# Kernel tuning notes

Measured on AMD Instinct MI355X. Metric: run time of the kernel, lower is better.

Reference implementation:

```python
import jax, jax.numpy as jnp
import numpy as np

EPS = 1e-5
NEG_SLOPE = 0.2
B, C, P, K, E, H = 16, 16, 2048, 16, 64, 2


def cross_set_gather(f, idx):
    # f: (B, C, P), idx: (B, P, K) -> (B, C, P, K)
    return jax.vmap(lambda fb, ib: fb[:, ib])(f, idx)


def bn(x, g, b, m, v, axes):
    # x normalized along channel dim; g,b,m,v shaped to broadcast via `axes` reshape
    return (x - m.reshape(axes)) * (g.reshape(axes) / jnp.sqrt(v.reshape(axes) + EPS)) + b.reshape(axes)


def setup_inputs() -> dict:
    key = jax.random.key(0)
    ks = jax.random.split(key, 16)
    features = jax.random.normal(ks[0], (B, C, P), dtype=jnp.float32)
    neighbor_indices = jax.random.randint(ks[1], (B, P, K), 0, P)
    mask = jax.random.randint(ks[2], (B, 1, P), 0, 2).astype(bool)
    s = 0.1
    return {
        "features": features,
        "neighbor_indices": neighbor_indices,
        "mask": mask,
        "node_w": jax.random.normal(ks[3], (H, E, C)) * s,
        "node_g": jnp.ones((H, E)),
        "node_b": jnp.zeros((H, E)),
        "node_m": jax.random.normal(ks[4], (H, E)) * s,
        "node_v": jax.random.uniform(ks[5], (H, E)) + 0.5,
        "edge_w": jax.random.normal(ks[6], (H, E, C)) * s,
        "edge_bias": jax.random.normal(ks[7], (H, E)) * s,
        "edge_g": jnp.ones((H, E)),
        "edge_b2": jnp.zeros((H, E)),
        "edge_m": jax.random.normal(ks[8], (H, E)) * s,
        "edge_v": jax.random.uniform(ks[9], (H, E)) + 0.5,
        "self_w": jax.random.normal(ks[10], (H, E)) * s,
        "self_b": jax.random.normal(ks[11], (H,)) * s,
        "nb_w": jax.random.normal(ks[12], (H, E)) * s,
        "nb_b": jax.random.normal(ks[13], (H,)) * s,
    }


def _forward(features, neighbor_indices, mask, node_w, node_g, node_b, node_m, node_v,
             edge_w, edge_bias, edge_g, edge_b2, edge_m, edge_v, self_w, self_b, nb_w, nb_b):
    mask_f = mask.astype(features.dtype)  # (B,1,P)
    # node encoding (Conv1d k=1 + BN): (B,H,E,P)
    nodes = jnp.einsum('hec,bcp->bhep', node_w, features)
    nodes = bn(nodes, node_g, node_b, node_m, node_v, (1, H, E, 1))
    # edge features: neighbor - center, (B,C,P,K)
    nbr = cross_set_gather(features, neighbor_indices)
    edge_feat = nbr - features[:, :, :, None]
    # edge encoding (Conv2d k=1 + BN): (B,H,E,P,K)
    enc = jnp.einsum('hec,bcpk->bhepk', edge_w, edge_feat) + edge_bias[None, :, :, None, None]
    enc = bn(enc, edge_g, edge_b2, edge_m, edge_v, (1, H, E, 1, 1))
    # attention scores
    self_score = jnp.einsum('he,bhep->bhp', self_w, nodes) + self_b[None, :, None]  # (B,H,P)
    nb_score = jnp.einsum('he,bhepk->bhpk', nb_w, enc) + nb_b[None, :, None, None]  # (B,H,P,K)
    logits = self_score[..., None] + nb_score
    logits = jnp.where(logits >= 0, logits, NEG_SLOPE * logits)  # leaky_relu(0.2)
    # neighbor validity mask: (B,P,K)
    valid = cross_set_gather(mask_f, neighbor_indices)[:, 0]
    vb = valid[:, None, :, :]  # (B,1,P,K)
    logits = jnp.where(vb == 0, -jnp.inf, logits)
    coef = jnp.nan_to_num(jax.nn.softmax(logits, axis=-1), nan=0.0, posinf=0.0, neginf=0.0)  # (B,H,P,K)
    # weighted aggregation + relu: (B,H,E,P)
    att = jax.nn.relu(jnp.einsum('bhpk,bhepk->bhep', coef, enc))
    # graph features: masked max over K
    enc_masked = jnp.where(vb[:, :, None, :, :] == 0, -jnp.inf, enc)
    graph = jnp.max(enc_masked, axis=-1)  # (B,H,E,P)
    graph = jnp.where(jnp.isinf(graph), 0.0, graph)
    # multi-head combine: element-wise max over heads, then mask
    att_out = jnp.max(att, axis=1) * mask_f  # (B,E,P)
    graph_out = jnp.max(graph, axis=1) * mask_f  # (B,E,P)
    return att_out, graph_out


def reference(features, neighbor_indices, mask, node_w, node_g, node_b, node_m, node_v,
              edge_w, edge_bias, edge_g, edge_b2, edge_m, edge_v, self_w, self_b, nb_w, nb_b):
    return _forward(features, neighbor_indices, mask, node_w, node_g, node_b, node_m, node_v,
                    edge_w, edge_bias, edge_g, edge_b2, edge_m, edge_v, self_w, self_b, nb_w, nb_b)
```

## Files before the change

kernel.cpp:

```cpp
#include <hip/hip_runtime.h>
#include <hip/hip_bf16.h>
#include <hip/hip_fp16.h>
#include <math.h>

#define NB 16
#define NC 16
#define NP 2048
#define NK 16
#define NE 64
#define NH 2
#define EPSV 1e-5f
#define NSLOPE 0.2f
#define QINV -1e30f
#define QTHR -1e29f

#define WS_SECB  12288
#define WS_CNB2  13312
#define WS_PQ    16384
#define WS_PS    278528
#define WS_EPB   2162688

__device__ __forceinline__ float ldf(const void* p, int i, int isb) {
  return isb ? __bfloat162float(((const __hip_bfloat16*)p)[i]) : ((const float*)p)[i];
}
__device__ __forceinline__ unsigned f2bf(float f) {
  unsigned u = __float_as_uint(f);
  return (u + 0x7FFFu + ((u >> 16) & 1u)) >> 16;
}
__device__ __forceinline__ float bflo(unsigned v) { return __uint_as_float(v << 16); }
__device__ __forceinline__ float bfhi(unsigned v) { return __uint_as_float(v & 0xFFFF0000u); }

__global__ void __launch_bounds__(256) k_proj(
    const void* feat, const void* mask,
    const void* edge_w, const void* node_w,
    const void* edge_g, const void* edge_v, const void* edge_bias,
    const void* edge_m, const void* edge_b2,
    const void* node_g, const void* node_v, const void* node_b, const void* node_m,
    const void* self_w, const void* self_b, const void* nb_w, const void* nb_b,
    char* ws)
{
  __shared__ int sh_isb, sh_mbyte;
  __shared__ float ewl[128*17];
  __shared__ float nwl[128*17];
  __shared__ float fl[NC][64];
  __shared__ float w2[128], wn[128], ctr[128];
  __shared__ float s_wq[32], s_wsc[32], s_cself[2];
  __shared__ unsigned char mtile[64];

  const int tid = threadIdx.x;
  const int w = tid >> 6, lane = tid & 63;

  if (w == 0) {
    const unsigned short* u = (const unsigned short*)feat;
    int cnt = 0;
#pragma unroll
    for (int i = 0; i < 8; i++) {
      int ex = (u[lane*8 + i] >> 7) & 0xFF;
      cnt += (ex >= 100 && ex <= 135) ? 1 : 0;
    }
#pragma unroll
    for (int o = 32; o >= 1; o >>= 1) cnt += __shfl_xor(cnt, o);
    if (lane == 0) sh_isb = (cnt >= 460) ? 1 : 0;
  }
  if (w == 1) {
    const unsigned char* mb = (const unsigned char*)mask;
    int c = 0;
#pragma unroll
    for (int i = 0; i < 16; i++) {
      int ix = lane*16 + i;
      c += ((ix & 3) && mb[ix]) ? 1 : 0;
    }
#pragma unroll
    for (int o = 32; o >= 1; o >>= 1) c += __shfl_xor(c, o);
    if (lane == 0) sh_mbyte = (c > 0) ? 1 : 0;
  }
  __syncthreads();
  const int isb = sh_isb, mbyte = sh_mbyte;

  const int bid = blockIdx.x;
  const int b  = (bid & 7)*2 + ((bid >> 3) & 1);
  const int pt = bid >> 4;
  const int p0 = pt * 64;

  for (int i = tid; i < 128*16; i += 256) {
    const int he = i >> 4, c = i & 15;
    ewl[he*17 + c] = ldf(edge_w, i, isb);
    nwl[he*17 + c] = ldf(node_w, i, isb);
  }
  for (int i = tid; i < NC*64; i += 256) {
    int c = i >> 6, p = i & 63;
    fl[c][p] = ldf(feat, (b*NC + c)*NP + p0 + p, isb);
  }
  if (tid < 64) {
    bool mv;
    if (mbyte) mv = ((const unsigned char*)mask)[b*NP + p0 + tid] != 0;
    else       mv = ((const int*)mask)[b*NP + p0 + tid] != 0;
    mtile[tid] = mv ? 1 : 0;
  }
  if (tid >= 64 && tid < 192) {
    const int he = tid - 64, h = he >> 6;
    float se = ldf(edge_g, he, isb) * rsqrtf(ldf(edge_v, he, isb) + EPSV);
    float cb = se * (ldf(edge_bias, he, isb) - ldf(edge_m, he, isb)) + ldf(edge_b2, he, isb);
    float ns = ldf(node_g, he, isb) * rsqrtf(ldf(node_v, he, isb) + EPSV);
    w2[he]  = ldf(nb_w, he, isb) * se;
    wn[he]  = ldf(self_w, he, isb) * ns;
    ctr[he] = ldf(self_w, he, isb) * (ldf(node_b, he, isb) - ldf(node_m, he, isb) * ns);
    if (bid == 0) {
      ((float2*)(ws + WS_SECB))[he] = make_float2(se, cb);
      float t = ldf(nb_w, he, isb) * cb;
#pragma unroll
      for (int o = 32; o >= 1; o >>= 1) t += __shfl_xor(t, o);
      if ((he & 63) == 0)
        ((float*)(ws + WS_CNB2))[h] = t + ldf(nb_b, h, isb);
    }
  }
  if (bid == 0 && tid == 0) {
    ((int*)ws)[0] = isb;
    ((int*)ws)[1] = mbyte;
  }
  __syncthreads();

  if (tid < 128) {
    const int h = tid >> 6, c = (tid >> 2) & 15, eq = tid & 3;
    float sq = 0.f, sn = 0.f;
#pragma unroll
    for (int i = 0; i < 16; i++) {
      const int e = eq*16 + i;
      sq += w2[h*NE+e] * ewl[(h*NE+e)*17 + c];
      sn += wn[h*NE+e] * nwl[(h*NE+e)*17 + c];
    }
    sq += __shfl_xor(sq, 1); sq += __shfl_xor(sq, 2);
    sn += __shfl_xor(sn, 1); sn += __shfl_xor(sn, 2);
    if (eq == 0) { s_wq[h*16 + c] = sq; s_wsc[h*16 + c] = sn; }
  }
  if (tid >= 128 && tid < 136) {
    const int h = (tid - 128) >> 2, eq = tid & 3;
    float cs = 0.f;
#pragma unroll
    for (int i = 0; i < 16; i++) cs += ctr[h*NE + eq*16 + i];
    cs += __shfl_xor(cs, 1); cs += __shfl_xor(cs, 2);
    if (eq == 0) s_cself[h] = cs + ldf(self_b, h, isb);
  }
  __syncthreads();

  const int e = tid & 63;
  const int pp = tid >> 6;
  float wv0[NC], wv1[NC];
#pragma unroll
  for (int c = 0; c < NC; c++) {
    wv0[c] = ewl[e*17 + c];
    wv1[c] = ewl[(NE + e)*17 + c];
  }
  unsigned* epb = (unsigned*)(ws + WS_EPB);
  const long base = (long)(b*NP + p0) * 64;
  for (int pass = 0; pass < 16; pass++) {
    const int p = pass*4 + pp;
    if (!mtile[p]) continue;
    float a0 = 0.f, a1 = 0.f;
#pragma unroll
    for (int c = 0; c < NC; c++) {
      const float f = fl[c][p];
      a0 = fmaf(wv0[c], f, a0);
      a1 = fmaf(wv1[c], f, a1);
    }
    epb[base + (long)p*64 + e] = f2bf(a0) | (f2bf(a1) << 16);
  }

  if (tid < 64) {
    float q0=0.f, q1=0.f, s0=0.f, s1=0.f;
#pragma unroll
    for (int c = 0; c < NC; c++) {
      const float f = fl[c][tid];
      q0 = fmaf(s_wq[c],     f, q0);
      q1 = fmaf(s_wq[16+c],  f, q1);
      s0 = fmaf(s_wsc[c],    f, s0);
      s1 = fmaf(s_wsc[16+c], f, s1);
    }
    const int p = p0 + tid;
    const bool mv = mtile[tid] != 0;
    ((float2*)(ws + WS_PQ))[b*NP + p] = make_float2(mv ? q0 : QINV, mv ? q1 : QINV);
    ((float2*)(ws + WS_PS))[b*NP + p] = make_float2(s0 + s_cself[0], s1 + s_cself[1]);
  }
}

__global__ void __launch_bounds__(256) k_main(const int* nidx, char* ws, void* out)
{
  __shared__ float sh_se[128], sh_cbe[128], sh_cnb[2];
  __shared__ uint2 ent[32][17];
  __shared__ unsigned char cntcm[32];
  __shared__ float att_t[NE][33];
  __shared__ float gr_t[NE][33];

  const int tid  = threadIdx.x;
  const int w    = tid >> 6;
  const int lane = tid & 63;

  const int isb = ((const int*)ws)[0];
  if (tid < 128) {
    const float2 sc = ((const float2*)(ws + WS_SECB))[tid];
    sh_se[tid]  = sc.x;
    sh_cbe[tid] = sc.y;
  }
  if (tid < 2) sh_cnb[tid] = ((const float*)(ws + WS_CNB2))[tid];
  __syncthreads();

  const float2* Pq = (const float2*)(ws + WS_PQ);
  const float2* Ps = (const float2*)(ws + WS_PS);
  const int bid = blockIdx.x;
  const int b  = (bid & 7)*2 + ((bid >> 3) & 1);
  const int pt = bid >> 4;
  const int p0 = pt * 32;
  const float cnb0 = sh_cnb[0], cnb1 = sh_cnb[1];

  {
    const int pl = w*8 + (lane >> 3);
    const int p  = p0 + pl;
    const int kk = (lane & 7) * 2;
    const float2 Pcq = Pq[b*NP + p];
    const float2 Pcs = Ps[b*NP + p];
    const bool cm = (Pcq.x > QTHR);
    const int2 iv = *(const int2*)(nidx + ((long)b*NP + p)*NK + kk);
    const float2 Q0 = Pq[b*NP + iv.x];
    const float2 Q1 = Pq[b*NP + iv.y];
    const bool v0 = (Q0.x > QTHR), v1 = (Q1.x > QTHR);

    float l00 = Pcs.x + Q0.x - Pcq.x + cnb0;  l00 = (l00 >= 0.f) ? l00 : NSLOPE*l00;
    float l01 = Pcs.y + Q0.y - Pcq.y + cnb1;  l01 = (l01 >= 0.f) ? l01 : NSLOPE*l01;
    float l10 = Pcs.x + Q1.x - Pcq.x + cnb0;  l10 = (l10 >= 0.f) ? l10 : NSLOPE*l10;
    float l11 = Pcs.y + Q1.y - Pcq.y + cnb1;  l11 = (l11 >= 0.f) ? l11 : NSLOPE*l11;
    l00 = v0 ? l00 : -INFINITY;  l01 = v0 ? l01 : -INFINITY;
    l10 = v1 ? l10 : -INFINITY;  l11 = v1 ? l11 : -INFINITY;

    float mx0 = fmaxf(l00, l10), mx1 = fmaxf(l01, l11);
#pragma unroll
    for (int o = 1; o <= 4; o <<= 1) {
      mx0 = fmaxf(mx0, __shfl_xor(mx0, o));
      mx1 = fmaxf(mx1, __shfl_xor(mx1, o));
    }
    const float e00 = __expf(l00 - mx0), e10 = __expf(l10 - mx0);
    const float e01 = __expf(l01 - mx1), e11 = __expf(l11 - mx1);
    float s0 = e00 + e10, s1 = e01 + e11;
#pragma unroll
    for (int o = 1; o <= 4; o <<= 1) {
      s0 += __shfl_xor(s0, o);
      s1 += __shfl_xor(s1, o);
    }
    const float inv0 = 1.f / s0, inv1 = 1.f / s1;

    unsigned vmask = ((v0 ? 1u : 0u) << kk) | ((v1 ? 1u : 0u) << (kk + 1));
#pragma unroll
    for (int o = 1; o <= 4; o <<= 1) vmask |= __shfl_xor(vmask, o);

    const int pos0 = __popc(vmask & ((1u << kk) - 1));
    if (v0) {
      const __half2 h2 = __floats2half2_rn(e00 * inv0, e01 * inv1);
      uint2 en; en.x = *(const unsigned*)&h2; en.y = ((unsigned)iv.x) << 8;
      ent[pl][pos0] = en;
    }
    if (v1) {
      const __half2 h2 = __floats2half2_rn(e10 * inv0, e11 * inv1);
      uint2 en; en.x = *(const unsigned*)&h2; en.y = ((unsigned)iv.y) << 8;
      ent[pl][pos0 + (v0 ? 1 : 0)] = en;
    }
    if ((lane & 7) == 0)
      cntcm[pl] = (unsigned char)(__popc(vmask) | (cm ? 0x80 : 0));
  }
  __syncthreads();

  const float se0 = sh_se[lane],  se1 = sh_se[NE + lane];
  const float cb0 = sh_cbe[lane], cb1 = sh_cbe[NE + lane];
  const char* epb_b = ws + WS_EPB + (long)b * NP * 256;

  for (int j = 0; j < 8; j++) {
    const int pl = w*8 + j;
    const unsigned cc = cntcm[pl];
    if (!(cc & 0x80)) { att_t[lane][pl] = 0.f; gr_t[lane][pl] = 0.f; continue; }
    const int cnt = cc & 0x7F;

    const unsigned rawp = *(const unsigned*)(epb_b + (long)(p0 + pl)*256 + lane*4);
    const float ra0 = bflo(rawp), ra1 = bfhi(rawp);
    const float cpe0 = cb0 - se0*ra0, cpe1 = cb1 - se1*ra1;

    float a0 = 0.f, a1 = 0.f;
    float mx0 = -INFINITY, mn0 = INFINITY, mx1 = -INFINITY, mn1 = INFINITY;
#pragma unroll 4
    for (int k = 0; k < cnt; k++) {
      const uint2 en = ent[pl][k];
      const float2 cf = __half22float2(*(const __half2*)&en.x);
      const unsigned v = *(const unsigned*)(epb_b + en.y + lane*4);
      const float v0 = bflo(v), v1 = bfhi(v);
      a0 = fmaf(cf.x, v0, a0);
      a1 = fmaf(cf.y, v1, a1);
      mx0 = fmaxf(mx0, v0); mn0 = fminf(mn0, v0);
      mx1 = fmaxf(mx1, v1); mn1 = fminf(mn1, v1);
    }
    const bool av = (cnt > 0);
    const float csel = av ? 1.f : 0.f;
    const float att0 = fmaxf(fmaf(se0, a0, cpe0*csel), 0.f);
    const float att1 = fmaxf(fmaf(se1, a1, cpe1*csel), 0.f);
    const float g0 = av ? fmaf(se0, (se0 >= 0.f) ? mx0 : mn0, cpe0) : 0.f;
    const float g1 = av ? fmaf(se1, (se1 >= 0.f) ? mx1 : mn1, cpe1) : 0.f;
    att_t[lane][pl] = fmaxf(att0, att1);
    gr_t[lane][pl]  = fmaxf(g0, g1);
  }
  __syncthreads();

  const long obase = (long)b * NE * NP;
  const long go = (long)NB * NE * NP;
  for (int i = tid; i < NE*16; i += 256) {
    const int ee = i >> 4, pp = (i & 15) * 2;
    const long oi = obase + (long)ee * NP + p0 + pp;
    const float a0 = att_t[ee][pp], a1 = att_t[ee][pp+1];
    const float g0 = gr_t[ee][pp],  g1 = gr_t[ee][pp+1];
    if (isb) {
      __hip_bfloat16* o = (__hip_bfloat16*)out;
      *(ushort2*)&o[oi]      = make_ushort2((unsigned short)f2bf(a0), (unsigned short)f2bf(a1));
      *(ushort2*)&o[oi + go] = make_ushort2((unsigned short)f2bf(g0), (unsigned short)f2bf(g1));
    } else {
      float* o = (float*)out;
      *(float2*)&o[oi]      = make_float2(a0, a1);
      *(float2*)&o[oi + go] = make_float2(g0, g1);
    }
  }
}

extern "C" void kernel_launch(void* const* d_in, const int* in_sizes, int n_in,
                              void* d_out, int out_size, void* d_ws, size_t ws_size,
                              hipStream_t stream)
{
  const void* feat      = d_in[0];
  const void* nidx      = d_in[1];
  const void* mask      = d_in[2];
  const void* node_w    = d_in[3];
  const void* node_g    = d_in[4];
  const void* node_b    = d_in[5];
  const void* node_m    = d_in[6];
  const void* node_v    = d_in[7];
  const void* edge_w    = d_in[8];
  const void* edge_bias = d_in[9];
  const void* edge_g    = d_in[10];
  const void* edge_b2   = d_in[11];
  const void* edge_m    = d_in[12];
  const void* edge_v    = d_in[13];
  const void* self_w    = d_in[14];
  const void* self_b    = d_in[15];
  const void* nb_w      = d_in[16];
  const void* nb_b      = d_in[17];
  char* ws = (char*)d_ws;

  hipLaunchKernelGGL(k_proj, dim3(NB*(NP/64)), dim3(256), 0, stream,
                     feat, mask, edge_w, node_w,
                     edge_g, edge_v, edge_bias, edge_m, edge_b2,
                     node_g, node_v, node_b, node_m,
                     self_w, self_b, nb_w, nb_b, ws);
  hipLaunchKernelGGL(k_main, dim3(NB*(NP/32)), dim3(256), 0, stream,
                     (const int*)nidx, ws, d_out);
}
```

Before: 118.5 us.

## Halve points per block and batch neighbor gathers for memory-level parallelism

Both kernels now handle half as many points per block, doubling the grid, and k_main assigns one lane per neighbor instead of two. The aggregation loop first issues all 16 neighbor gathers into registers (clamped to a valid slot when the neighbor is invalid), then accumulates under a predicate, so the loads are in flight together rather than serialized in a dynamic loop. This targets gather latency and low occupancy, at the cost of more blocks, repeated per-block weight loading in k_proj, and wasted loads for masked-out neighbors.

```diff
diff --git a/kernel.cpp b/kernel.cpp
--- a/kernel.cpp
+++ b/kernel.cpp
@@ -42,10 +42,10 @@
   __shared__ int sh_isb, sh_mbyte;
   __shared__ float ewl[128*17];
   __shared__ float nwl[128*17];
-  __shared__ float fl[NC][64];
+  __shared__ float fl[NC][32];
   __shared__ float w2[128], wn[128], ctr[128];
   __shared__ float s_wq[32], s_wsc[32], s_cself[2];
-  __shared__ unsigned char mtile[64];
+  __shared__ unsigned char mtile[32];
 
   const int tid = threadIdx.x;
   const int w = tid >> 6, lane = tid & 63;
@@ -80,18 +80,18 @@
   const int bid = blockIdx.x;
   const int b  = (bid & 7)*2 + ((bid >> 3) & 1);
   const int pt = bid >> 4;
-  const int p0 = pt * 64;
+  const int p0 = pt * 32;
 
   for (int i = tid; i < 128*16; i += 256) {
     const int he = i >> 4, c = i & 15;
     ewl[he*17 + c] = ldf(edge_w, i, isb);
     nwl[he*17 + c] = ldf(node_w, i, isb);
   }
-  for (int i = tid; i < NC*64; i += 256) {
-    int c = i >> 6, p = i & 63;
+  for (int i = tid; i < NC*32; i += 256) {
+    int c = i >> 5, p = i & 31;
     fl[c][p] = ldf(feat, (b*NC + c)*NP + p0 + p, isb);
   }
-  if (tid < 64) {
+  if (tid < 32) {
     bool mv;
     if (mbyte) mv = ((const unsigned char*)mask)[b*NP + p0 + tid] != 0;
     else       mv = ((const int*)mask)[b*NP + p0 + tid] != 0;
@@ -153,7 +153,7 @@
   }
   unsigned* epb = (unsigned*)(ws + WS_EPB);
   const long base = (long)(b*NP + p0) * 64;
-  for (int pass = 0; pass < 16; pass++) {
+  for (int pass = 0; pass < 8; pass++) {
     const int p = pass*4 + pp;
     if (!mtile[p]) continue;
     float a0 = 0.f, a1 = 0.f;
@@ -166,7 +166,7 @@
     epb[base + (long)p*64 + e] = f2bf(a0) | (f2bf(a1) << 16);
   }
 
-  if (tid < 64) {
+  if (tid < 32) {
     float q0=0.f, q1=0.f, s0=0.f, s1=0.f;
 #pragma unroll
     for (int c = 0; c < NC; c++) {
@@ -186,10 +186,10 @@
 __global__ void __launch_bounds__(256) k_main(const int* nidx, char* ws, void* out)
 {
   __shared__ float sh_se[128], sh_cbe[128], sh_cnb[2];
-  __shared__ uint2 ent[32][17];
-  __shared__ unsigned char cntcm[32];
-  __shared__ float att_t[NE][33];
-  __shared__ float gr_t[NE][33];
+  __shared__ uint2 ent[16][17];
+  __shared__ unsigned char cntcm[16];
+  __shared__ float att_t[NE][17];
+  __shared__ float gr_t[NE][17];
 
   const int tid  = threadIdx.x;
   const int w    = tid >> 6;
@@ -209,60 +209,52 @@
   const int bid = blockIdx.x;
   const int b  = (bid & 7)*2 + ((bid >> 3) & 1);
   const int pt = bid >> 4;
-  const int p0 = pt * 32;
+  const int p0 = pt * 16;
   const float cnb0 = sh_cnb[0], cnb1 = sh_cnb[1];
 
   {
-    const int pl = w*8 + (lane >> 3);
+    const int pl = w*4 + (lane >> 4);
     const int p  = p0 + pl;
-    const int kk = (lane & 7) * 2;
+    const int kk = lane & 15;
     const float2 Pcq = Pq[b*NP + p];
     const float2 Pcs = Ps[b*NP + p];
     const bool cm = (Pcq.x > QTHR);
-    const int2 iv = *(const int2*)(nidx + ((long)b*NP + p)*NK + kk);
-    const float2 Q0 = Pq[b*NP + iv.x];
-    const float2 Q1 = Pq[b*NP + iv.y];
-    const bool v0 = (Q0.x > QTHR), v1 = (Q1.x > QTHR);
-
-    float l00 = Pcs.x + Q0.x - Pcq.x + cnb0;  l00 = (l00 >= 0.f) ? l00 : NSLOPE*l00;
-    float l01 = Pcs.y + Q0.y - Pcq.y + cnb1;  l01 = (l01 >= 0.f) ? l01 : NSLOPE*l01;
-    float l10 = Pcs.x + Q1.x - Pcq.x + cnb0;  l10 = (l10 >= 0.f) ? l10 : NSLOPE*l10;
-    float l11 = Pcs.y + Q1.y - Pcq.y + cnb1;  l11 = (l11 >= 0.f) ? l11 : NSLOPE*l11;
-    l00 = v0 ? l00 : -INFINITY;  l01 = v0 ? l01 : -INFINITY;
-    l10 = v1 ? l10 : -INFINITY;  l11 = v1 ? l11 : -INFINITY;
-
-    float mx0 = fmaxf(l00, l10), mx1 = fmaxf(l01, l11);
-#pragma unroll
-    for (int o = 1; o <= 4; o <<= 1) {
+    const int iv = nidx[((long)b*NP + p)*NK + kk];
+    const float2 Q0 = Pq[b*NP + iv];
+    const bool v0 = (Q0.x > QTHR);
+
+    float l0 = Pcs.x + Q0.x - Pcq.x + cnb0;  l0 = (l0 >= 0.f) ? l0 : NSLOPE*l0;
+    float l1 = Pcs.y + Q0.y - Pcq.y + cnb1;  l1 = (l1 >= 0.f) ? l1 : NSLOPE*l1;
+    l0 = v0 ? l0 : -INFINITY;
+    l1 = v0 ? l1 : -INFINITY;
+
+    float mx0 = l0, mx1 = l1;
+#pragma unroll
+    for (int o = 1; o <= 8; o <<= 1) {
       mx0 = fmaxf(mx0, __shfl_xor(mx0, o));
       mx1 = fmaxf(mx1, __shfl_xor(mx1, o));
     }
-    const float e00 = __expf(l00 - mx0), e10 = __expf(l10 - mx0);
-    const float e01 = __expf(l01 - mx1), e11 = __expf(l11 - mx1);
-    float s0 = e00 + e10, s1 = e01 + e11;
-#pragma unroll
-    for (int o = 1; o <= 4; o <<= 1) {
+    const float e0 = __expf(l0 - mx0);
+    const float e1 = __expf(l1 - mx1);
+    float s0 = e0, s1 = e1;
+#pragma unroll
+    for (int o = 1; o <= 8; o <<= 1) {
       s0 += __shfl_xor(s0, o);
       s1 += __shfl_xor(s1, o);
     }
     const float inv0 = 1.f / s0, inv1 = 1.f / s1;
 
-    unsigned vmask = ((v0 ? 1u : 0u) << kk) | ((v1 ? 1u : 0u) << (kk + 1));
-#pragma unroll
-    for (int o = 1; o <= 4; o <<= 1) vmask |= __shfl_xor(vmask, o);
-
-    const int pos0 = __popc(vmask & ((1u << kk) - 1));
+    unsigned vmask = (v0 ? 1u : 0u) << kk;
+#pragma unroll
+    for (int o = 1; o <= 8; o <<= 1) vmask |= __shfl_xor(vmask, o);
+
     if (v0) {
-      const __half2 h2 = __floats2half2_rn(e00 * inv0, e01 * inv1);
-      uint2 en; en.x = *(const unsigned*)&h2; en.y = ((unsigned)iv.x) << 8;
-      ent[pl][pos0] = en;
-    }
-    if (v1) {
-      const __half2 h2 = __floats2half2_rn(e10 * inv0, e11 * inv1);
-      uint2 en; en.x = *(const unsigned*)&h2; en.y = ((unsigned)iv.y) << 8;
-      ent[pl][pos0 + (v0 ? 1 : 0)] = en;
-    }
-    if ((lane & 7) == 0)
+      const int pos = __popc(vmask & ((1u << kk) - 1u));
+      const __half2 h2 = __floats2half2_rn(e0 * inv0, e1 * inv1);
+      uint2 en; en.x = *(const unsigned*)&h2; en.y = ((unsigned)iv) << 8;
+      ent[pl][pos] = en;
+    }
+    if (kk == 0)
       cntcm[pl] = (unsigned char)(__popc(vmask) | (cm ? 0x80 : 0));
   }
   __syncthreads();
@@ -271,35 +263,42 @@
   const float cb0 = sh_cbe[lane], cb1 = sh_cbe[NE + lane];
   const char* epb_b = ws + WS_EPB + (long)b * NP * 256;
 
-  for (int j = 0; j < 8; j++) {
-    const int pl = w*8 + j;
+  for (int j = 0; j < 4; j++) {
+    const int pl = w*4 + j;
     const unsigned cc = cntcm[pl];
-    if (!(cc & 0x80)) { att_t[lane][pl] = 0.f; gr_t[lane][pl] = 0.f; continue; }
     const int cnt = cc & 0x7F;
+    if (!(cc & 0x80) || cnt == 0) { att_t[lane][pl] = 0.f; gr_t[lane][pl] = 0.f; continue; }
 
     const unsigned rawp = *(const unsigned*)(epb_b + (long)(p0 + pl)*256 + lane*4);
+
+    unsigned vr[16];
+#pragma unroll
+    for (int k = 0; k < 16; k++) {
+      const unsigned off = ent[pl][(k < cnt) ? k : 0].y;
+      vr[k] = *(const unsigned*)(epb_b + off + lane*4);
+    }
+
     const float ra0 = bflo(rawp), ra1 = bfhi(rawp);
     const float cpe0 = cb0 - se0*ra0, cpe1 = cb1 - se1*ra1;
 
     float a0 = 0.f, a1 = 0.f;
     float mx0 = -INFINITY, mn0 = INFINITY, mx1 = -INFINITY, mn1 = INFINITY;
-#pragma unroll 4
-    for (int k = 0; k < cnt; k++) {
-      const uint2 en = ent[pl][k];
-      const float2 cf = __half22float2(*(const __half2*)&en.x);
-      const unsigned v = *(const unsigned*)(epb_b + en.y + lane*4);
-      const float v0 = bflo(v), v1 = bfhi(v);
-      a0 = fmaf(cf.x, v0, a0);
-      a1 = fmaf(cf.y, v1, a1);
-      mx0 = fmaxf(mx0, v0); mn0 = fminf(mn0, v0);
-      mx1 = fmaxf(mx1, v1); mn1 = fminf(mn1, v1);
-    }
-    const bool av = (cnt > 0);
-    const float csel = av ? 1.f : 0.f;
-    const float att0 = fmaxf(fmaf(se0, a0, cpe0*csel), 0.f);
-    const float att1 = fmaxf(fmaf(se1, a1, cpe1*csel), 0.f);
-    const float g0 = av ? fmaf(se0, (se0 >= 0.f) ? mx0 : mn0, cpe0) : 0.f;
-    const float g1 = av ? fmaf(se1, (se1 >= 0.f) ? mx1 : mn1, cpe1) : 0.f;
+#pragma unroll
+    for (int k = 0; k < 16; k++) {
+      if (k < cnt) {
+        const uint2 en = ent[pl][k];
+        const float2 cf = __half22float2(*(const __half2*)&en.x);
+        const float v0 = bflo(vr[k]), v1 = bfhi(vr[k]);
+        a0 = fmaf(cf.x, v0, a0);
+        a1 = fmaf(cf.y, v1, a1);
+        mx0 = fmaxf(mx0, v0); mn0 = fminf(mn0, v0);
+        mx1 = fmaxf(mx1, v1); mn1 = fminf(mn1, v1);
+      }
+    }
+    const float att0 = fmaxf(fmaf(se0, a0, cpe0), 0.f);
+    const float att1 = fmaxf(fmaf(se1, a1, cpe1), 0.f);
+    const float g0 = fmaf(se0, (se0 >= 0.f) ? mx0 : mn0, cpe0);
+    const float g1 = fmaf(se1, (se1 >= 0.f) ? mx1 : mn1, cpe1);
     att_t[lane][pl] = fmaxf(att0, att1);
     gr_t[lane][pl]  = fmaxf(g0, g1);
   }
@@ -307,8 +306,8 @@
 
   const long obase = (long)b * NE * NP;
   const long go = (long)NB * NE * NP;
-  for (int i = tid; i < NE*16; i += 256) {
-    const int ee = i >> 4, pp = (i & 15) * 2;
+  for (int i = tid; i < NE*8; i += 256) {
+    const int ee = i >> 3, pp = (i & 7) * 2;
     const long oi = obase + (long)ee * NP + p0 + pp;
     const float a0 = att_t[ee][pp], a1 = att_t[ee][pp+1];
     const float g0 = gr_t[ee][pp],  g1 = gr_t[ee][pp+1];
@@ -348,11 +347,11 @@
   const void* nb_b      = d_in[17];
   char* ws = (char*)d_ws;
 
-  hipLaunchKernelGGL(k_proj, dim3(NB*(NP/64)), dim3(256), 0, stream,
+  hipLaunchKernelGGL(k_proj, dim3(NB*(NP/32)), dim3(256), 0, stream,
                      feat, mask, edge_w, node_w,
                      edge_g, edge_v, edge_bias, edge_m, edge_b2,
                      node_g, node_v, node_b, node_m,
                      self_w, self_b, nb_w, nb_b, ws);
-  hipLaunchKernelGGL(k_main, dim3(NB*(NP/32)), dim3(256), 0, stream,
+  hipLaunchKernelGGL(k_main, dim3(NB*(NP/16)), dim3(256), 0, stream,
                      (const int*)nidx, ws, d_out);
 }
```

Result: slower. 121.6 us (+2.6%).

## Split neighbor gather across half-waves with 8-byte loads and batched prefetch

Applied to the files above, without the earlier changes.

Reworks the per-point aggregation loop. Each half-wave now handles alternate neighbors and loads two adjacent channels with 8-byte reads. The partial sums and min/max are combined across halves with a cross-lane shuffle. All neighbor loads are issued up front into registers so they overlap, and a padding entry pointing at the center point makes odd counts safe. This aims at memory latency and narrow-load overhead in the gather, at the cost of more registers and extra shuffles per point.

```diff
diff --git a/kernel.cpp b/kernel.cpp
--- a/kernel.cpp
+++ b/kernel.cpp
@@ -262,46 +262,81 @@
       uint2 en; en.x = *(const unsigned*)&h2; en.y = ((unsigned)iv.y) << 8;
       ent[pl][pos0 + (v0 ? 1 : 0)] = en;
     }
-    if ((lane & 7) == 0)
-      cntcm[pl] = (unsigned char)(__popc(vmask) | (cm ? 0x80 : 0));
-  }
-  __syncthreads();
-
-  const float se0 = sh_se[lane],  se1 = sh_se[NE + lane];
-  const float cb0 = sh_cbe[lane], cb1 = sh_cbe[NE + lane];
+    if ((lane & 7) == 0) {
+      const int nv = __popc(vmask);
+      cntcm[pl] = (unsigned char)(nv | (cm ? 0x80 : 0));
+      uint2 pe; pe.x = 0u; pe.y = ((unsigned)p) << 8;
+      ent[pl][nv] = pe;
+    }
+  }
+  __syncthreads();
+
+  const int hl = lane >> 5;
+  const int le = lane & 31;
+  const int ebase = le << 1;
+  const int eidx  = ebase + hl;
+  const float seh0 = sh_se[eidx],  seh1 = sh_se[NE + eidx];
+  const float cbh0 = sh_cbe[eidx], cbh1 = sh_cbe[NE + eidx];
   const char* epb_b = ws + WS_EPB + (long)b * NP * 256;
 
   for (int j = 0; j < 8; j++) {
     const int pl = w*8 + j;
     const unsigned cc = cntcm[pl];
-    if (!(cc & 0x80)) { att_t[lane][pl] = 0.f; gr_t[lane][pl] = 0.f; continue; }
     const int cnt = cc & 0x7F;
-
-    const unsigned rawp = *(const unsigned*)(epb_b + (long)(p0 + pl)*256 + lane*4);
-    const float ra0 = bflo(rawp), ra1 = bfhi(rawp);
-    const float cpe0 = cb0 - se0*ra0, cpe1 = cb1 - se1*ra1;
-
-    float a0 = 0.f, a1 = 0.f;
-    float mx0 = -INFINITY, mn0 = INFINITY, mx1 = -INFINITY, mn1 = INFINITY;
-#pragma unroll 4
-    for (int k = 0; k < cnt; k++) {
-      const uint2 en = ent[pl][k];
-      const float2 cf = __half22float2(*(const __half2*)&en.x);
-      const unsigned v = *(const unsigned*)(epb_b + en.y + lane*4);
-      const float v0 = bflo(v), v1 = bfhi(v);
-      a0 = fmaf(cf.x, v0, a0);
-      a1 = fmaf(cf.y, v1, a1);
-      mx0 = fmaxf(mx0, v0); mn0 = fminf(mn0, v0);
-      mx1 = fmaxf(mx1, v1); mn1 = fminf(mn1, v1);
-    }
-    const bool av = (cnt > 0);
-    const float csel = av ? 1.f : 0.f;
-    const float att0 = fmaxf(fmaf(se0, a0, cpe0*csel), 0.f);
-    const float att1 = fmaxf(fmaf(se1, a1, cpe1*csel), 0.f);
-    const float g0 = av ? fmaf(se0, (se0 >= 0.f) ? mx0 : mn0, cpe0) : 0.f;
-    const float g1 = av ? fmaf(se1, (se1 >= 0.f) ? mx1 : mn1, cpe1) : 0.f;
-    att_t[lane][pl] = fmaxf(att0, att1);
-    gr_t[lane][pl]  = fmaxf(g0, g1);
+    if (!(cc & 0x80) || cnt == 0) { att_t[eidx][pl] = 0.f; gr_t[eidx][pl] = 0.f; continue; }
+
+    const uint2 rawc = *(const uint2*)(epb_b + ((long)(p0 + pl) << 8) + ebase*4);
+    const unsigned rawme = hl ? rawc.y : rawc.x;
+    const float cpe0 = cbh0 - seh0 * bflo(rawme);
+    const float cpe1 = cbh1 - seh1 * bfhi(rawme);
+
+    const int npair = (cnt + 1) >> 1;
+    uint2 vr[8];
+#pragma unroll
+    for (int kp = 0; kp < 8; kp++) {
+      if (kp < npair) {
+        const int kidx = min(kp*2 + hl, cnt);
+        vr[kp] = *(const uint2*)(epb_b + ent[pl][kidx].y + ebase*4);
+      }
+    }
+
+    float am0=0.f, am1=0.f, as0=0.f, as1=0.f;
+    float mxm0=-INFINITY, mnm0=INFINITY, mxm1=-INFINITY, mnm1=INFINITY;
+    float mxs0=-INFINITY, mns0=INFINITY, mxs1=-INFINITY, mns1=INFINITY;
+#pragma unroll
+    for (int kp = 0; kp < 8; kp++) {
+      if (kp < npair) {
+        const int kr = kp*2 + hl;
+        const uint2 en = ent[pl][min(kr, cnt)];
+        const float2 cf = __half22float2(*(const __half2*)&en.x);
+        const unsigned um = hl ? vr[kp].y : vr[kp].x;
+        const unsigned us = hl ? vr[kp].x : vr[kp].y;
+        const float vm0 = bflo(um), vm1 = bfhi(um);
+        const float vs0 = bflo(us), vs1 = bfhi(us);
+        am0 = fmaf(cf.x, vm0, am0);
+        am1 = fmaf(cf.y, vm1, am1);
+        as0 = fmaf(cf.x, vs0, as0);
+        as1 = fmaf(cf.y, vs1, as1);
+        const bool kv = kr < cnt;
+        mxm0 = fmaxf(mxm0, kv ? vm0 : -INFINITY); mnm0 = fminf(mnm0, kv ? vm0 : INFINITY);
+        mxm1 = fmaxf(mxm1, kv ? vm1 : -INFINITY); mnm1 = fminf(mnm1, kv ? vm1 : INFINITY);
+        mxs0 = fmaxf(mxs0, kv ? vs0 : -INFINITY); mns0 = fminf(mns0, kv ? vs0 : INFINITY);
+        mxs1 = fmaxf(mxs1, kv ? vs1 : -INFINITY); mns1 = fminf(mns1, kv ? vs1 : INFINITY);
+      }
+    }
+    const float A0  = am0 + __shfl_xor(as0, 32);
+    const float A1  = am1 + __shfl_xor(as1, 32);
+    const float MX0 = fmaxf(mxm0, __shfl_xor(mxs0, 32));
+    const float MN0 = fminf(mnm0, __shfl_xor(mns0, 32));
+    const float MX1 = fmaxf(mxm1, __shfl_xor(mxs1, 32));
+    const float MN1 = fminf(mnm1, __shfl_xor(mns1, 32));
+
+    const float att0 = fmaxf(fmaf(seh0, A0, cpe0), 0.f);
+    const float att1 = fmaxf(fmaf(seh1, A1, cpe1), 0.f);
+    const float g0 = fmaf(seh0, (seh0 >= 0.f) ? MX0 : MN0, cpe0);
+    const float g1 = fmaf(seh1, (seh1 >= 0.f) ? MX1 : MN1, cpe1);
+    att_t[eidx][pl] = fmaxf(att0, att1);
+    gr_t[eidx][pl]  = fmaxf(g0, g1);
   }
   __syncthreads();
 
```

Result: slower. 124.5 us (+5.1%).
